# Kernel tuning notes

Hardware: AMD Instinct MI355X
Metric: run time of the kernel (lower is better)

Reference implementation:

```python
import jax, jax.numpy as jnp
import numpy as np

EPS = 1e-5


def _adabin_act_quant_1bit(x):
    # AdabinQuantizer, num_bits=1, layerwise=False, beta=0 (fresh zeros param).
    # alpha: per-sample scale, detached: 2*mean|x - beta| / sqrt(Qp=1), shape (N,1,1,1)
    alpha = jax.lax.stop_gradient(2.0 * jnp.mean(jnp.abs(x), axis=(1, 2, 3), keepdims=True))
    alpha = jnp.maximum(alpha, EPS)
    # forward: alpha * sign(x); STE grad: pass-through where |x/alpha| <= 1 (clip grad)
    clipped = jnp.clip(x / alpha, -1.0, 1.0)
    return alpha * (clipped + jax.lax.stop_gradient(jnp.sign(x) - clipped))


def _bwn_weight_quant(w):
    # BwnQuantizer, layerwise=False: per-output-channel L1 mean scale,
    # w_q = sign(w) * m, STE backward = identity.
    m = jnp.mean(jnp.abs(w), axis=(1, 2, 3), keepdims=True)  # (O,1,1,1)
    return w + jax.lax.stop_gradient(jnp.sign(w) * m - w)


def setup_inputs() -> dict:
    key = jax.random.key(0)
    kx, kw = jax.random.split(key)
    x = jax.random.normal(kx, (32, 256, 56, 56), dtype=jnp.float32)
    weight = jax.random.normal(kw, (256, 256, 3, 3), dtype=jnp.float32) * 0.05
    return {"x": x, "weight": weight}


def reference(x, weight):
    xq = _adabin_act_quant_1bit(x)
    wq = _bwn_weight_quant(weight)
    out = jax.lax.conv_general_dilated(
        xq, wq,
        window_strides=(1, 1),
        padding=((1, 1), (1, 1)),
        dimension_numbers=("NCHW", "OIHW", "NCHW"),
    )
    return out
```

## Files before the change

### kernel.cpp

```cpp
#include <hip/hip_runtime.h>
#include <cstdint>

typedef int   i32x4 __attribute__((ext_vector_type(4)));
typedef int   i32x8 __attribute__((ext_vector_type(8)));
typedef float f32x4 __attribute__((ext_vector_type(4)));

static constexpr int N_IMG = 32, HWP = 3136, KK = 2304, HP = 58;
static constexpr size_t XPAD_BYTES = (size_t)N_IMG * HP * HP * 256;
static constexpr size_t OFF_XPAD = 0;
static constexpr size_t OFF_WSGN = XPAD_BYTES;
static constexpr size_t OFF_MSC  = OFF_WSGN + (size_t)256 * KK;
static constexpr size_t OFF_ACC  = OFF_MSC + 1024;

__device__ __forceinline__ void async16(const void* g, const void* l) {
    __builtin_amdgcn_global_load_lds(
        (const __attribute__((address_space(1))) uint32_t*)g,
        (__attribute__((address_space(3))) uint32_t*)l, 16, 0, 0);
}

__device__ __forceinline__ unsigned char sign_fp8(float v) {
    return (v > 0.f) ? 0x38u : ((v < 0.f) ? 0xB8u : 0u);
}

__device__ __forceinline__ int xoff(int kt) {
    int rs = kt >> 1, rr = rs / 3, ss = rs - rr * 3;
    return (rr * HP + ss) * 256 + ((kt & 1) << 7);
}

__global__ __launch_bounds__(256) void k_wm(const float* __restrict__ w,
                                            unsigned char* __restrict__ wA,
                                            float* __restrict__ msc,
                                            float* __restrict__ acc32) {
    int ko = blockIdx.x, t = threadIdx.x;
    __shared__ unsigned char s[2304];
    __shared__ float red[4];
    float sum = 0.f;
    #pragma unroll
    for (int i = 0; i < 9; ++i) {
        float v = w[(size_t)ko * KK + i * 256 + t];
        sum += fabsf(v);
        s[i * 256 + t] = sign_fp8(v);
    }
    #pragma unroll
    for (int off = 32; off; off >>= 1) sum += __shfl_down(sum, off, 64);
    if ((t & 63) == 0) red[t >> 6] = sum;
    __syncthreads();
    if (t == 0) msc[ko] = (red[0] + red[1] + red[2] + red[3]) * (1.f / 2304.f);
    if (ko == 0 && t < 32) acc32[t] = 0.f;
    #pragma unroll
    for (int i = 0; i < 9; ++i)
        wA[((size_t)(i * 2 + (t >> 7)) * 256 + ko) * 128 + (t & 127)] = s[t * 9 + i];
}

__global__ __launch_bounds__(256) void k_xpad(const float* __restrict__ x,
                                              unsigned char* __restrict__ xpad,
                                              float* __restrict__ acc32) {
    int bx = blockIdx.x, n = blockIdx.y;
    int t = threadIdx.x;
    {
        int g = (n * 49 + bx) * 256 + t;
        if (g < 32 * 228 * 16) {
            int n2 = g / 3648, rem = g - n2 * 3648;
            int pos = rem >> 4, j = rem & 15;
            int h, wq;
            if (pos < 58)       { h = 0;         wq = pos; }
            else if (pos < 116) { h = 57;        wq = pos - 58; }
            else if (pos < 172) { h = pos - 115; wq = 0; }
            else                { h = pos - 171; wq = 57; }
            *(i32x4*)&xpad[(((size_t)n2 * HP + h) * HP + wq) * 256 + j * 16] =
                (i32x4){0, 0, 0, 0};
        }
    }
    int hw0 = bx * 64;
    int cg = t & 15, hwg = t >> 4;
    int c16 = cg * 16;
    int hwb = hw0 + hwg * 4;

    f32x4 v[16];
    #pragma unroll
    for (int jc = 0; jc < 16; ++jc)
        v[jc] = *(const f32x4*)&x[((size_t)(n * 256 + c16 + jc)) * HWP + hwb];

    float asum = 0.f;
    #pragma unroll
    for (int jc = 0; jc < 16; ++jc)
        #pragma unroll
        for (int k = 0; k < 4; ++k) asum += fabsf(v[jc][k]);

    int h = hwb / 56, wp = hwb - h * 56;
    unsigned char* dst = &xpad[(((size_t)n * HP + h + 1) * HP + (wp + 1)) * 256 + c16];
    #pragma unroll
    for (int k = 0; k < 4; ++k) {
        i32x4 pk;
        #pragma unroll
        for (int q = 0; q < 4; ++q) {
            pk[q] = (int)((unsigned)sign_fp8(v[4 * q + 0][k])
                        | ((unsigned)sign_fp8(v[4 * q + 1][k]) << 8)
                        | ((unsigned)sign_fp8(v[4 * q + 2][k]) << 16)
                        | ((unsigned)sign_fp8(v[4 * q + 3][k]) << 24));
        }
        *(i32x4*)(dst + (size_t)k * 256) = pk;
    }

    #pragma unroll
    for (int off = 32; off; off >>= 1) asum += __shfl_down(asum, off, 64);
    __shared__ float red[4];
    if ((t & 63) == 0) red[t >> 6] = asum;
    __syncthreads();
    if (t == 0) atomicAdd(&acc32[n], red[0] + red[1] + red[2] + red[3]);
}

__global__ __launch_bounds__(256, 3) void k_gemm(const unsigned char* __restrict__ wA,
                                                 const unsigned char* __restrict__ xpad,
                                                 const float* __restrict__ acc32,
                                                 const float* __restrict__ msc,
                                                 float* __restrict__ out) {
    __shared__ __attribute__((aligned(16))) unsigned char Wt[128 * 128];
    __shared__ __attribute__((aligned(16))) unsigned char Xt[128 * 128];
    const int t = threadIdx.x;
    const int lane = t & 63, wv = t >> 6;
    const int mtile = blockIdx.x, ntile = blockIdx.y;
    const int quad = lane >> 4, r16 = lane & 15;
    const int wm = wv & 1, wn = wv >> 1;

    const int lrow = lane >> 3;
    const int pxs  = (lane & 7) ^ lrow;
    const int kc   = ((pxs & 3) << 1) | (pxs >> 2);

    const unsigned char* wp[4];
    const unsigned char* xp[4];
    unsigned char* ldsW[4];
    unsigned char* ldsX[4];
    #pragma unroll
    for (int rnd = 0; rnd < 4; ++rnd) {
        int row = (wv * 4 + rnd) * 8 + lrow;
        wp[rnd] = wA + (size_t)(mtile * 128 + row) * 128 + kc * 16;
        int p = ntile * 128 + row;
        int nimg = p / HWP, hw = p - nimg * HWP;
        int h = hw / 56, wpos = hw - h * 56;
        xp[rnd] = xpad + (((size_t)nimg * HP + h) * HP + wpos) * 256 + kc * 16;
        ldsW[rnd] = Wt + (wv * 4 + rnd) * 1024;
        ldsX[rnd] = Xt + (wv * 4 + rnd) * 1024;
    }

    f32x4 acc[4][4];
    #pragma unroll
    for (int i = 0; i < 4; ++i)
        #pragma unroll
        for (int j = 0; j < 4; ++j)
            acc[i][j] = (f32x4){0.f, 0.f, 0.f, 0.f};

    for (int kt = 0; kt < 18; ++kt) {
        const size_t offW = (size_t)kt * 32768;
        const int offX = xoff(kt);
        #pragma unroll
        for (int rnd = 0; rnd < 4; ++rnd) async16(wp[rnd] + offW, ldsW[rnd]);
        #pragma unroll
        for (int rnd = 0; rnd < 4; ++rnd) async16(xp[rnd] + offX, ldsX[rnd]);
        asm volatile("s_waitcnt vmcnt(0)" ::: "memory");
        __syncthreads();

        i32x8 b8[4];
        #pragma unroll
        for (int j = 0; j < 4; ++j) {
            int row = wn * 64 + j * 16 + r16, sw = row & 7;
            i32x4 lo = *(const i32x4*)(Xt + row * 128 + ((quad ^ sw) << 4));
            i32x4 hi = *(const i32x4*)(Xt + row * 128 + (((quad | 4) ^ sw) << 4));
            b8[j] = __builtin_shufflevector(lo, hi, 0, 1, 2, 3, 4, 5, 6, 7);
        }
        #pragma unroll
        for (int i = 0; i < 4; ++i) {
            int row = wm * 64 + i * 16 + r16, sw = row & 7;
            i32x4 lo = *(const i32x4*)(Wt + row * 128 + ((quad ^ sw) << 4));
            i32x4 hi = *(const i32x4*)(Wt + row * 128 + (((quad | 4) ^ sw) << 4));
            i32x8 a8 = __builtin_shufflevector(lo, hi, 0, 1, 2, 3, 4, 5, 6, 7);
            #pragma unroll
            for (int j = 0; j < 4; ++j)
                acc[i][j] = __builtin_amdgcn_mfma_scale_f32_16x16x128_f8f6f4(
                    a8, b8[j], acc[i][j], 0, 0, 0, 127, 0, 127);
        }
        __syncthreads();
    }

    float mscv[4][4];
    #pragma unroll
    for (int i = 0; i < 4; ++i) {
        int ko0 = mtile * 128 + wm * 64 + i * 16 + quad * 4;
        #pragma unroll
        for (int r = 0; r < 4; ++r) mscv[i][r] = msc[ko0 + r];
    }
    #pragma unroll
    for (int j = 0; j < 4; ++j) {
        int p = ntile * 128 + wn * 64 + j * 16 + r16;
        int nimg = p / HWP, hw = p - nimg * HWP;
        float av = fmaxf(acc32[nimg] * (2.f / 802816.f), 1e-5f);
        float* outp = out + (size_t)nimg * 802816 + hw;
        #pragma unroll
        for (int i = 0; i < 4; ++i) {
            int ko0 = mtile * 128 + wm * 64 + i * 16 + quad * 4;
            #pragma unroll
            for (int r = 0; r < 4; ++r)
                outp[(size_t)(ko0 + r) * HWP] = acc[i][j][r] * av * mscv[i][r];
        }
    }
}

extern "C" void kernel_launch(void* const* d_in, const int* in_sizes, int n_in,
                              void* d_out, int out_size, void* d_ws, size_t ws_size,
                              hipStream_t stream) {
    const float* x = (const float*)d_in[0];
    const float* w = (const float*)d_in[1];
    float* out = (float*)d_out;
    char* ws = (char*)d_ws;
    unsigned char* xpad = (unsigned char*)(ws + OFF_XPAD);
    unsigned char* wA   = (unsigned char*)(ws + OFF_WSGN);
    float* msc   = (float*)(ws + OFF_MSC);
    float* acc32 = (float*)(ws + OFF_ACC);

    k_wm<<<256, 256, 0, stream>>>(w, wA, msc, acc32);
    k_xpad<<<dim3(49, N_IMG), 256, 0, stream>>>(x, xpad, acc32);
    k_gemm<<<dim3(2, 784), 256, 0, stream>>>(wA, xpad, acc32, msc, out);
}
```

Before: 249.1 us.

## Widen GEMM tile to all 256 output channels per block

```diff
diff --git a/kernel.cpp b/kernel.cpp
--- a/kernel.cpp
+++ b/kernel.cpp
@@ -115,69 +115,74 @@
                                                  const float* __restrict__ acc32,
                                                  const float* __restrict__ msc,
                                                  float* __restrict__ out) {
-    __shared__ __attribute__((aligned(16))) unsigned char Wt[128 * 128];
+    __shared__ __attribute__((aligned(16))) unsigned char Wt[256 * 128];
     __shared__ __attribute__((aligned(16))) unsigned char Xt[128 * 128];
     const int t = threadIdx.x;
     const int lane = t & 63, wv = t >> 6;
-    const int mtile = blockIdx.x, ntile = blockIdx.y;
+    const int ntile = blockIdx.x;
     const int quad = lane >> 4, r16 = lane & 15;
-    const int wm = wv & 1, wn = wv >> 1;
 
     const int lrow = lane >> 3;
     const int pxs  = (lane & 7) ^ lrow;
     const int kc   = ((pxs & 3) << 1) | (pxs >> 2);
 
-    const unsigned char* wp[4];
+    const unsigned char* wp[8];
+    unsigned char* ldsW[8];
+    #pragma unroll
+    for (int rnd = 0; rnd < 8; ++rnd) {
+        int s = wv * 8 + rnd;
+        int row = s * 8 + lrow;
+        wp[rnd] = wA + (size_t)row * 128 + kc * 16;
+        ldsW[rnd] = Wt + s * 1024;
+    }
     const unsigned char* xp[4];
-    unsigned char* ldsW[4];
     unsigned char* ldsX[4];
     #pragma unroll
     for (int rnd = 0; rnd < 4; ++rnd) {
-        int row = (wv * 4 + rnd) * 8 + lrow;
-        wp[rnd] = wA + (size_t)(mtile * 128 + row) * 128 + kc * 16;
+        int s = wv * 4 + rnd;
+        int row = s * 8 + lrow;
         int p = ntile * 128 + row;
         int nimg = p / HWP, hw = p - nimg * HWP;
         int h = hw / 56, wpos = hw - h * 56;
         xp[rnd] = xpad + (((size_t)nimg * HP + h) * HP + wpos) * 256 + kc * 16;
-        ldsW[rnd] = Wt + (wv * 4 + rnd) * 1024;
-        ldsX[rnd] = Xt + (wv * 4 + rnd) * 1024;
-    }
-
-    f32x4 acc[4][4];
+        ldsX[rnd] = Xt + s * 1024;
+    }
+
+    f32x4 acc[4][8];
     #pragma unroll
     for (int i = 0; i < 4; ++i)
         #pragma unroll
-        for (int j = 0; j < 4; ++j)
+        for (int j = 0; j < 8; ++j)
             acc[i][j] = (f32x4){0.f, 0.f, 0.f, 0.f};
 
     for (int kt = 0; kt < 18; ++kt) {
         const size_t offW = (size_t)kt * 32768;
         const int offX = xoff(kt);
         #pragma unroll
-        for (int rnd = 0; rnd < 4; ++rnd) async16(wp[rnd] + offW, ldsW[rnd]);
+        for (int rnd = 0; rnd < 8; ++rnd) async16(wp[rnd] + offW, ldsW[rnd]);
         #pragma unroll
         for (int rnd = 0; rnd < 4; ++rnd) async16(xp[rnd] + offX, ldsX[rnd]);
         asm volatile("s_waitcnt vmcnt(0)" ::: "memory");
         __syncthreads();
 
-        i32x8 b8[4];
-        #pragma unroll
-        for (int j = 0; j < 4; ++j) {
-            int row = wn * 64 + j * 16 + r16, sw = row & 7;
+        i32x8 a8[4];
+        #pragma unroll
+        for (int i = 0; i < 4; ++i) {
+            int row = wv * 64 + i * 16 + r16, sw = row & 7;
+            i32x4 lo = *(const i32x4*)(Wt + row * 128 + ((quad ^ sw) << 4));
+            i32x4 hi = *(const i32x4*)(Wt + row * 128 + (((quad | 4) ^ sw) << 4));
+            a8[i] = __builtin_shufflevector(lo, hi, 0, 1, 2, 3, 4, 5, 6, 7);
+        }
+        #pragma unroll
+        for (int j = 0; j < 8; ++j) {
+            int row = j * 16 + r16, sw = row & 7;
             i32x4 lo = *(const i32x4*)(Xt + row * 128 + ((quad ^ sw) << 4));
             i32x4 hi = *(const i32x4*)(Xt + row * 128 + (((quad | 4) ^ sw) << 4));
-            b8[j] = __builtin_shufflevector(lo, hi, 0, 1, 2, 3, 4, 5, 6, 7);
-        }
-        #pragma unroll
-        for (int i = 0; i < 4; ++i) {
-            int row = wm * 64 + i * 16 + r16, sw = row & 7;
-            i32x4 lo = *(const i32x4*)(Wt + row * 128 + ((quad ^ sw) << 4));
-            i32x4 hi = *(const i32x4*)(Wt + row * 128 + (((quad | 4) ^ sw) << 4));
-            i32x8 a8 = __builtin_shufflevector(lo, hi, 0, 1, 2, 3, 4, 5, 6, 7);
+            i32x8 b8 = __builtin_shufflevector(lo, hi, 0, 1, 2, 3, 4, 5, 6, 7);
             #pragma unroll
-            for (int j = 0; j < 4; ++j)
+            for (int i = 0; i < 4; ++i)
                 acc[i][j] = __builtin_amdgcn_mfma_scale_f32_16x16x128_f8f6f4(
-                    a8, b8[j], acc[i][j], 0, 0, 0, 127, 0, 127);
+                    a8[i], b8, acc[i][j], 0, 0, 0, 127, 0, 127);
         }
         __syncthreads();
     }
@@ -185,19 +190,19 @@
     float mscv[4][4];
     #pragma unroll
     for (int i = 0; i < 4; ++i) {
-        int ko0 = mtile * 128 + wm * 64 + i * 16 + quad * 4;
+        int ko0 = wv * 64 + i * 16 + quad * 4;
         #pragma unroll
         for (int r = 0; r < 4; ++r) mscv[i][r] = msc[ko0 + r];
     }
     #pragma unroll
-    for (int j = 0; j < 4; ++j) {
-        int p = ntile * 128 + wn * 64 + j * 16 + r16;
+    for (int j = 0; j < 8; ++j) {
+        int p = ntile * 128 + j * 16 + r16;
         int nimg = p / HWP, hw = p - nimg * HWP;
         float av = fmaxf(acc32[nimg] * (2.f / 802816.f), 1e-5f);
         float* outp = out + (size_t)nimg * 802816 + hw;
         #pragma unroll
         for (int i = 0; i < 4; ++i) {
-            int ko0 = mtile * 128 + wm * 64 + i * 16 + quad * 4;
+            int ko0 = wv * 64 + i * 16 + quad * 4;
             #pragma unroll
             for (int r = 0; r < 4; ++r)
                 outp[(size_t)(ko0 + r) * HWP] = acc[i][j][r] * av * mscv[i][r];
@@ -219,5 +224,5 @@
 
     k_wm<<<256, 256, 0, stream>>>(w, wA, msc, acc32);
     k_xpad<<<dim3(49, N_IMG), 256, 0, stream>>>(x, xpad, acc32);
-    k_gemm<<<dim3(2, 784), 256, 0, stream>>>(wA, xpad, acc32, msc, out);
-}
+    k_gemm<<<784, 256, 0, stream>>>(wA, xpad, acc32, msc, out);
+}
```

Result: slower. 393.0 us (+57.8%).
